# Kernel tuning notes

Measured on AMD Instinct MI355X. Metric: run time of the kernel, lower is better.

The kernel has to match this reference:

```python
import jax, jax.numpy as jnp
import numpy as np

P_DROP = 0.3
TEMP = 1.0
UNC_THRESH = 0.3
TOP_K = 2
EXTRA_K = 2  # min(2, num_experts - top_k)
NUM_SAMPLES = 5


def setup_inputs() -> dict:
    key = jax.random.key(0)
    ks = jax.random.split(key, 7)
    B, D, H, E = 16384, 4096, 128, 64
    return {
        "x": jax.random.normal(ks[0], (B, D), jnp.float32),
        "W1": jax.random.normal(ks[1], (D, H), jnp.float32) / np.sqrt(D),
        "b1": jnp.zeros((H,), jnp.float32),
        "W2": jax.random.normal(ks[2], (H, E), jnp.float32) / np.sqrt(H),
        "b2": jnp.zeros((E,), jnp.float32),
        "mask1_u": jax.random.uniform(ks[3], (NUM_SAMPLES, B, H), jnp.float32),
        "mask2_u": jax.random.uniform(ks[4], (NUM_SAMPLES, B, E), jnp.float32),
    }


def reference(x, W1, b1, W2, b2, mask1_u, mask2_u):
    scale = 1.0 / (1.0 - P_DROP)
    # layer1: Linear -> ReLU -> Dropout; W1 is shared, so compute once and
    # apply per-sample dropout masks (identical math to the torch loop).
    h = jax.nn.relu(x @ W1 + b1)                              # [B, H]
    h = h[None] * ((mask1_u >= P_DROP).astype(h.dtype) * scale)  # [S, B, H]
    # layer2: Linear -> Dropout
    logits = jnp.einsum("sbh,he->sbe", h, W2) + b2            # [S, B, E]
    logits = logits * ((mask2_u >= P_DROP).astype(logits.dtype) * scale)

    mean_logits = logits.mean(axis=0)                          # [B, E]
    probs = jax.nn.softmax(mean_logits / TEMP, axis=-1)        # [B, E]
    all_probs = jax.nn.softmax(logits / TEMP, axis=-1)         # [S, B, E]
    # torch .std() is unbiased (ddof=1)
    uncertainty = jnp.std(all_probs, axis=0, ddof=1).mean(axis=-1)  # [B]

    # top_k + conditional expansion by EXTRA_K when uncertain.
    full_probs, full_idx = jax.lax.top_k(probs, TOP_K + EXTRA_K)
    topk_probs, topk_idx = full_probs[:, :TOP_K], full_idx[:, :TOP_K]
    uncertain = (uncertainty > UNC_THRESH)[:, None]
    extra_probs = jnp.where(uncertain, full_probs[:, TOP_K:], 0.0)
    extra_idx = jnp.where(uncertain, full_idx[:, TOP_K:], -1)
    out_idx = jnp.concatenate([topk_idx, extra_idx], axis=1)       # [B, TOP_K+EXTRA_K]
    out_probs = jnp.concatenate([topk_probs, extra_probs], axis=1)
    return out_idx, out_probs, uncertainty
```

## Files before the change

### kernel.cpp

```cpp
#include <hip/hip_runtime.h>

typedef short short8 __attribute__((ext_vector_type(8)));
typedef short short4v __attribute__((ext_vector_type(4)));
typedef float f32x4 __attribute__((ext_vector_type(4)));

#define B_ROWS 16384
#define SCALE 1.4285714285714286f

__device__ __forceinline__ float bf2f(unsigned short u) {
    return __uint_as_float(((unsigned)u) << 16);
}
__device__ __forceinline__ unsigned short f2bf(float f) {
    unsigned u = __float_as_uint(f);
    u += 0x7fffu + ((u >> 16) & 1u);
    return (unsigned short)(u >> 16);
}

__device__ __forceinline__ void gl_lds16(const void* g, void* l) {
    __builtin_amdgcn_global_load_lds(
        (const __attribute__((address_space(1))) unsigned int*)g,
        (__attribute__((address_space(3))) unsigned int*)l, 16, 0, 0);
}

__device__ __forceinline__ float wave_max(float v) {
    #pragma unroll
    for (int m = 1; m < 64; m <<= 1) v = fmaxf(v, __shfl_xor(v, m, 64));
    return v;
}
__device__ __forceinline__ float wave_sum(float v) {
    #pragma unroll
    for (int m = 1; m < 64; m <<= 1) v += __shfl_xor(v, m, 64);
    return v;
}

__global__ void k_prep(const float* __restrict__ w1,
                       unsigned short* __restrict__ w1h,
                       unsigned short* __restrict__ w1l) {
    int tid = blockIdx.x * 256 + threadIdx.x;
    int n = tid >> 12, k = tid & 4095;
    float v = w1[k * 128 + n];
    unsigned short hi = f2bf(v);
    w1h[tid] = hi;
    w1l[tid] = f2bf(v - bf2f(hi));
}

__global__ __launch_bounds__(512, 4) void k_fused(
        const float* __restrict__ x,
        const unsigned short* __restrict__ w1h,
        const unsigned short* __restrict__ w1l,
        const float* __restrict__ b1,
        const float* __restrict__ w2,
        const float* __restrict__ b2,
        const float* __restrict__ m1,
        const float* __restrict__ m2,
        float* __restrict__ out) {
    __shared__ __attribute__((aligned(128))) char smem[81920];
    unsigned short* sAh0 = (unsigned short*)smem;
    unsigned short* sAl0 = (unsigned short*)(smem + 8192);
    unsigned short* sBh0 = (unsigned short*)(smem + 16384);
    unsigned short* sBl0 = (unsigned short*)(smem + 49152);
    float* hbuf = (float*)smem;
    float* lgs  = (float*)(smem + 16384);

    const int t = threadIdx.x;
    const int w = t >> 6, lane = t & 63;
    const int l15 = lane & 15, l4 = lane >> 4;
    const int rowBase = blockIdx.x << 5;

    const int am = t >> 4;
    const int rem = t & 15;
    const int aDst = (((am << 3) + ((rem >> 1) ^ (am & 7))) << 3) + ((rem & 1) << 2);

    f32x4 acc[2];
    #pragma unroll
    for (int mf = 0; mf < 2; ++mf) {
        f32x4 z = {0.f, 0.f, 0.f, 0.f};
        acc[mf] = z;
    }

    auto stageB = [&](int buf, int k0) {
        #pragma unroll
        for (int j = 0; j < 2; ++j) {
            int c = (j << 9) + t;
            int n = c >> 3;
            int cl = (c & 7) ^ (n & 7);
            const size_t go = (size_t)n * 4096 + k0 + (cl << 3);
            gl_lds16(w1h + go, sBh0 + (buf << 13) + (c << 3));
            gl_lds16(w1l + go, sBl0 + (buf << 13) + (c << 3));
        }
    };
    auto loadA = [&](int k0) {
        return *(const float4*)(x + ((size_t)(rowBase + am) << 12) + k0 + (rem << 2));
    };
    auto writeA = [&](int buf, float4 a0) {
        float av[4] = {a0.x, a0.y, a0.z, a0.w};
        short4v H, L;
        #pragma unroll
        for (int i = 0; i < 4; ++i) {
            unsigned short hi = f2bf(av[i]);
            H[i] = (short)hi;
            L[i] = (short)f2bf(av[i] - bf2f(hi));
        }
        *(short4v*)(sAh0 + (buf << 11) + aDst) = H;
        *(short4v*)(sAl0 + (buf << 11) + aDst) = L;
    };

    stageB(0, 0);
    writeA(0, loadA(0));
    __syncthreads();

    for (int it = 0; it < 64; ++it) {
        const int buf = it & 1;
        const bool pf = (it + 1 < 64);
        float4 aN = make_float4(0.f, 0.f, 0.f, 0.f);
        if (pf) {
            stageB(buf ^ 1, (it + 1) << 6);
            aN = loadA((it + 1) << 6);
        }
        #pragma unroll
        for (int ks = 0; ks < 2; ++ks) {
            short8 ah[2], al[2], bh, bl;
            #pragma unroll
            for (int mf = 0; mf < 2; ++mf) {
                int rm = (mf << 4) + l15;
                int pc = ((ks << 2) + l4) ^ (rm & 7);
                int o = ((rm << 3) + pc) << 3;
                ah[mf] = *(const short8*)(sAh0 + (buf << 11) + o);
                al[mf] = *(const short8*)(sAl0 + (buf << 11) + o);
            }
            {
                int rn = (w << 4) + l15;
                int pc = ((ks << 2) + l4) ^ (rn & 7);
                int o = ((rn << 3) + pc) << 3;
                bh = *(const short8*)(sBh0 + (buf << 13) + o);
                bl = *(const short8*)(sBl0 + (buf << 13) + o);
            }
            #pragma unroll
            for (int mf = 0; mf < 2; ++mf) {
                acc[mf] = __builtin_amdgcn_mfma_f32_16x16x32_bf16(ah[mf], bh, acc[mf], 0, 0, 0);
                acc[mf] = __builtin_amdgcn_mfma_f32_16x16x32_bf16(ah[mf], bl, acc[mf], 0, 0, 0);
                acc[mf] = __builtin_amdgcn_mfma_f32_16x16x32_bf16(al[mf], bh, acc[mf], 0, 0, 0);
            }
        }
        if (pf) writeA(buf ^ 1, aN);
        __syncthreads();
    }

    {
        const int col = (w << 4) + l15;
        const float bias = b1[col];
        #pragma unroll
        for (int mf = 0; mf < 2; ++mf) {
            const int rbase = (mf << 4) + (l4 << 2);
            #pragma unroll
            for (int rr = 0; rr < 4; ++rr) {
                const int r = rbase + rr;
                float v = acc[mf][rr] + bias;
                v = v > 0.f ? v : 0.f;
                hbuf[r * 128 + (col ^ ((r & 7) << 2))] = v;
            }
        }
    }
    __syncthreads();

    const int lr = t >> 4;
    const int eg = t & 15;
    const int e0 = eg << 2;
    const int row = rowBase + lr;
    const int lsw = (lr & 7) << 2;

    float acc2[5][4];
    #pragma unroll
    for (int s = 0; s < 5; ++s)
        #pragma unroll
        for (int e = 0; e < 4; ++e) acc2[s][e] = 0.f;

    const float* hrow = hbuf + lr * 128;
    const size_t m1row = ((size_t)row) << 7;

    for (int k = 0; k < 128; k += 4) {
        float4 h4 = *(const float4*)(hrow + (k ^ lsw));
        float hv[4] = {h4.x, h4.y, h4.z, h4.w};
        float w2v[4][4];
        #pragma unroll
        for (int kk = 0; kk < 4; ++kk) {
            float4 wa = *(const float4*)(w2 + ((k + kk) << 6) + e0);
            w2v[kk][0] = wa.x; w2v[kk][1] = wa.y; w2v[kk][2] = wa.z; w2v[kk][3] = wa.w;
        }
        #pragma unroll
        for (int s = 0; s < 5; ++s) {
            float4 mu = *(const float4*)(m1 + (size_t)s * (B_ROWS * 128) + m1row + k);
            float hd[4];
            hd[0] = (mu.x >= 0.3f) ? hv[0] * SCALE : 0.f;
            hd[1] = (mu.y >= 0.3f) ? hv[1] * SCALE : 0.f;
            hd[2] = (mu.z >= 0.3f) ? hv[2] * SCALE : 0.f;
            hd[3] = (mu.w >= 0.3f) ? hv[3] * SCALE : 0.f;
            #pragma unroll
            for (int kk = 0; kk < 4; ++kk)
                #pragma unroll
                for (int e = 0; e < 4; ++e)
                    acc2[s][e] += hd[kk] * w2v[kk][e];
        }
    }

    {
        float4 ba = *(const float4*)(b2 + e0);
        float bv4[4] = {ba.x, ba.y, ba.z, ba.w};
        #pragma unroll
        for (int s = 0; s < 5; ++s) {
            const float* m2p = m2 + ((size_t)s * B_ROWS + row) * 64 + e0;
            float4 ma = *(const float4*)m2p;
            float mk[4] = {ma.x, ma.y, ma.z, ma.w};
            float lv[4];
            #pragma unroll
            for (int e = 0; e < 4; ++e) {
                float v = acc2[s][e] + bv4[e];
                lv[e] = (mk[e] >= 0.3f) ? v * SCALE : 0.f;
            }
            *(float4*)(lgs + ((s << 5) + lr) * 64 + e0) =
                make_float4(lv[0], lv[1], lv[2], lv[3]);
        }
    }
    __syncthreads();

    for (int r4 = 0; r4 < 4; ++r4) {
        const int r = (w << 2) + r4;
        float l[5], p[5];
        #pragma unroll
        for (int s = 0; s < 5; ++s)
            l[s] = lgs[((s << 5) + r) * 64 + lane];

        float ml = ((((l[0] + l[1]) + l[2]) + l[3]) + l[4]) / 5.0f;

        #pragma unroll
        for (int s = 0; s < 5; ++s) {
            float mx = wave_max(l[s]);
            float ev = expf(l[s] - mx);
            float sm = wave_sum(ev);
            p[s] = ev / sm;
        }

        float mx = wave_max(ml);
        float ev = expf(ml - mx);
        float sm = wave_sum(ev);
        float prob = ev / sm;

        float mean = ((((p[0] + p[1]) + p[2]) + p[3]) + p[4]) / 5.0f;
        float var = 0.f;
        #pragma unroll
        for (int s = 0; s < 5; ++s) { float d = p[s] - mean; var += d * d; }
        float sd = sqrtf(var * 0.25f);
        float unc = wave_sum(sd) / 64.0f;

        float pv = prob;
        float vv[4]; int vi[4];
        #pragma unroll
        for (int q = 0; q < 4; ++q) {
            float bvx = pv; int bi = lane;
            #pragma unroll
            for (int m = 1; m < 64; m <<= 1) {
                float ov = __shfl_xor(bvx, m, 64);
                int oi = __shfl_xor(bi, m, 64);
                if (ov > bvx || (ov == bvx && oi < bi)) { bvx = ov; bi = oi; }
            }
            vv[q] = bvx; vi[q] = bi;
            if (lane == bi) pv = -1.f;
        }

        if (lane == 0) {
            int grow = rowBase + r;
            bool ug = unc > 0.3f;
            float4 fi = make_float4((float)vi[0], (float)vi[1],
                                    ug ? (float)vi[2] : -1.f,
                                    ug ? (float)vi[3] : -1.f);
            *(float4*)(out + (size_t)grow * 4) = fi;
            float4 fp = make_float4(vv[0], vv[1],
                                    ug ? vv[2] : 0.f,
                                    ug ? vv[3] : 0.f);
            *(float4*)(out + 65536 + (size_t)grow * 4) = fp;
            out[131072 + grow] = unc;
        }
    }
}

extern "C" void kernel_launch(void* const* d_in, const int* in_sizes, int n_in,
                              void* d_out, int out_size, void* d_ws, size_t ws_size,
                              hipStream_t stream) {
    const float* x  = (const float*)d_in[0];
    const float* W1 = (const float*)d_in[1];
    const float* b1 = (const float*)d_in[2];
    const float* W2 = (const float*)d_in[3];
    const float* b2 = (const float*)d_in[4];
    const float* m1 = (const float*)d_in[5];
    const float* m2 = (const float*)d_in[6];
    float* out = (float*)d_out;
    char* ws = (char*)d_ws;

    unsigned short* w1h = (unsigned short*)ws;
    unsigned short* w1l = (unsigned short*)(ws + (1 << 20));

    k_prep <<<2048, 256, 0, stream>>>(W1, w1h, w1l);
    k_fused<<<512,  512, 0, stream>>>(x, w1h, w1l, b1, W2, b2, m1, m2, out);
}
```

Before: 484.0 us.

## Stage masked hidden activations and W2 in LDS for the second-layer GEMV

Before, every thread loaded its own dropout-mask float4s from global memory, repeated across the 16 threads sharing a row, and read W2 from global memory on every k step. Now the block loads the masks cooperatively and coalesced, applies them to h, and writes masked h for two samples at a time into double slots in LDS. W2 is also copied once into LDS. The inner loop then reads only from LDS and reuses each W2 fragment for two samples, at the cost of extra __syncthreads between sample pairs and runtime-indexed accumulators that could spill if the outer loop is not unrolled.

```diff
diff --git a/kernel.cpp b/kernel.cpp
--- a/kernel.cpp
+++ b/kernel.cpp
@@ -60,6 +60,8 @@
     unsigned short* sBh0 = (unsigned short*)(smem + 16384);
     unsigned short* sBl0 = (unsigned short*)(smem + 49152);
     float* hbuf = (float*)smem;
+    float* hmb  = (float*)(smem + 16384);
+    float* w2s  = (float*)(smem + 49152);
     float* lgs  = (float*)(smem + 16384);
 
     const int t = threadIdx.x;
@@ -175,31 +177,68 @@
         #pragma unroll
         for (int e = 0; e < 4; ++e) acc2[s][e] = 0.f;
 
-    const float* hrow = hbuf + lr * 128;
-    const size_t m1row = ((size_t)row) << 7;
-
-    for (int k = 0; k < 128; k += 4) {
-        float4 h4 = *(const float4*)(hrow + (k ^ lsw));
-        float hv[4] = {h4.x, h4.y, h4.z, h4.w};
-        float w2v[4][4];
-        #pragma unroll
-        for (int kk = 0; kk < 4; ++kk) {
-            float4 wa = *(const float4*)(w2 + ((k + kk) << 6) + e0);
-            w2v[kk][0] = wa.x; w2v[kk][1] = wa.y; w2v[kk][2] = wa.z; w2v[kk][3] = wa.w;
-        }
-        #pragma unroll
-        for (int s = 0; s < 5; ++s) {
-            float4 mu = *(const float4*)(m1 + (size_t)s * (B_ROWS * 128) + m1row + k);
-            float hd[4];
-            hd[0] = (mu.x >= 0.3f) ? hv[0] * SCALE : 0.f;
-            hd[1] = (mu.y >= 0.3f) ? hv[1] * SCALE : 0.f;
-            hd[2] = (mu.z >= 0.3f) ? hv[2] * SCALE : 0.f;
-            hd[3] = (mu.w >= 0.3f) ? hv[3] * SCALE : 0.f;
+    auto stage_hm = [&](int slot, int sidx) {
+        #pragma unroll
+        for (int j = 0; j < 2; ++j) {
+            int q = t + (j << 9);
+            int r = q >> 5, kq = q & 31;
+            float4 mu = *(const float4*)(m1 + (size_t)sidx * (B_ROWS * 128)
+                                            + (((size_t)(rowBase + r)) << 7) + (kq << 2));
+            int off = r * 128 + ((kq << 2) ^ ((r & 7) << 2));
+            float4 h4 = *(const float4*)(hbuf + off);
+            float4 hm4;
+            hm4.x = (mu.x >= 0.3f) ? h4.x * SCALE : 0.f;
+            hm4.y = (mu.y >= 0.3f) ? h4.y * SCALE : 0.f;
+            hm4.z = (mu.z >= 0.3f) ? h4.z * SCALE : 0.f;
+            hm4.w = (mu.w >= 0.3f) ? h4.w * SCALE : 0.f;
+            *(float4*)(hmb + (slot << 12) + off) = hm4;
+        }
+    };
+
+    #pragma unroll
+    for (int j = 0; j < 4; ++j) {
+        int q = t + (j << 9);
+        *(float4*)(w2s + (q << 2)) = *(const float4*)(w2 + (q << 2));
+    }
+    stage_hm(0, 0);
+    stage_hm(1, 1);
+    __syncthreads();
+
+    for (int p = 0; p < 3; ++p) {
+        const int s0 = p << 1;
+        const int ns = (p == 2) ? 1 : 2;
+        const float* hm0 = hmb + lr * 128;
+        const float* hm1 = hmb + 4096 + lr * 128;
+        for (int kq = 0; kq < 32; ++kq) {
+            const int hoff = (kq << 2) ^ lsw;
+            float4 a0 = *(const float4*)(hm0 + hoff);
+            float ha[4] = {a0.x, a0.y, a0.z, a0.w};
+            float w2v[4][4];
+            #pragma unroll
+            for (int kk = 0; kk < 4; ++kk) {
+                float4 wa = *(const float4*)(w2s + (((kq << 2) + kk) << 6) + e0);
+                w2v[kk][0] = wa.x; w2v[kk][1] = wa.y; w2v[kk][2] = wa.z; w2v[kk][3] = wa.w;
+            }
             #pragma unroll
             for (int kk = 0; kk < 4; ++kk)
                 #pragma unroll
                 for (int e = 0; e < 4; ++e)
-                    acc2[s][e] += hd[kk] * w2v[kk][e];
+                    acc2[s0][e] += ha[kk] * w2v[kk][e];
+            if (ns == 2) {
+                float4 a1 = *(const float4*)(hm1 + hoff);
+                float hb[4] = {a1.x, a1.y, a1.z, a1.w};
+                #pragma unroll
+                for (int kk = 0; kk < 4; ++kk)
+                    #pragma unroll
+                    for (int e = 0; e < 4; ++e)
+                        acc2[s0 + 1][e] += hb[kk] * w2v[kk][e];
+            }
+        }
+        __syncthreads();
+        if (p < 2) {
+            stage_hm(0, (p << 1) + 2);
+            if (p == 0) stage_hm(1, 3);
+            __syncthreads();
         }
     }
 
```

Result: faster. 470.1 us (-2.9%).
